# Performance work log

Hardware: AMD Instinct MI355X
Metric: run time of the kernel (lower is better)

## Reference

```python
import jax, jax.numpy as jnp
import numpy as np
from jax import lax

# dims per init_kwargs / input_specs
V, D, N, W, B, T = 32000, 512, 250000, 64, 4, 1024
LOOPS, THRESH = 4, 0.99


def _ln(x, scale, bias):
    m = jnp.mean(x, -1, keepdims=True)
    v = jnp.var(x, -1, keepdims=True)
    return (x - m) * lax.rsqrt(v + 1e-5) * scale + bias


def setup_inputs() -> dict:
    key = jax.random.key(0)
    ks = jax.random.split(key, 12)
    s = 0.02
    p = lambda k, shape: jax.random.normal(k, shape, jnp.float32) * s
    return {
        "input_ids": jax.random.randint(ks[0], (B, T), 0, V),
        "embed": p(ks[1], (V, D)),
        "enc_w": p(ks[2], (D, D)), "enc_b": jnp.zeros((D,), jnp.float32),
        "ln_enc_s": jnp.ones((D,), jnp.float32), "ln_enc_b": jnp.zeros((D,), jnp.float32),
        "idx_w": p(ks[3], (D, D)), "idx_b": jnp.zeros((D,), jnp.float32),
        "mu_w": p(ks[4], (D, 1)), "mu_b": jnp.zeros((1,), jnp.float32),
        "sig_w": p(ks[5], (D, 1)), "sig_b": jnp.zeros((1,), jnp.float32),
        "pool_table": p(ks[6], (N, D)),
        "int_w1": p(ks[7], (2 * D, D)), "int_b1": jnp.zeros((D,), jnp.float32),
        "int_w2": p(ks[8], (D, D)), "int_b2": jnp.zeros((D,), jnp.float32),
        "ln_s": jnp.ones((D,), jnp.float32), "ln_b": jnp.zeros((D,), jnp.float32),
        "halt_w": p(ks[9], (D, 1)), "halt_b": jnp.zeros((1,), jnp.float32),
        "dec_w": p(ks[10], (D, V)), "dec_b": jnp.zeros((V,), jnp.float32),
    }


def reference(input_ids, embed, enc_w, enc_b, ln_enc_s, ln_enc_b,
              idx_w, idx_b, mu_w, mu_b, sig_w, sig_b, pool_table,
              int_w1, int_b1, int_w2, int_b2, ln_s, ln_b,
              halt_w, halt_b, dec_w, dec_b):
    # TinyController.encode: embed -> Dense -> gelu -> LayerNorm
    hidden = _ln(jax.nn.gelu(embed[input_ids] @ enc_w + enc_b), ln_enc_s, ln_enc_b)  # [B,T,D]
    state = hidden
    dt = hidden.dtype
    halt_prob = jnp.zeros((B, T, 1), dt)
    halted = jnp.zeros((B, T, 1), dt)
    idxs = []
    for _ in range(LOOPS):  # fixed small loop count, unrolled
        prev = state
        pooled = jnp.mean(state, axis=1)                       # [B,D]
        h = jax.nn.gelu(pooled @ idx_w + idx_b)
        mu = jax.nn.sigmoid(h @ mu_w + mu_b)                   # [B,1], coord in [0,1]
        sigma = jax.nn.softplus(h @ sig_w + sig_b) + 1e-4      # [B,1]
        # CoordinateMassivePool: contiguous window of W rows around mu*N
        center = mu[:, 0] * N
        start = jnp.clip(jnp.floor(center - W / 2).astype(jnp.int32), 0, N - W)  # [B]
        window = jax.vmap(lambda s: lax.dynamic_slice(pool_table, (s, 0), (W, D)))(start)  # [B,W,D]
        pos = (start[:, None] + jnp.arange(W)[None, :]).astype(dt) / N            # [B,W]
        w = jnp.exp(-0.5 * ((pos - mu) / sigma) ** 2)
        w = w / jnp.sum(w, axis=-1, keepdims=True)
        retrieved = jnp.einsum('bw,bwd->bd', w, window)        # [B,D]
        combined = jnp.concatenate(
            [state, jnp.broadcast_to(retrieved[:, None, :], (B, T, D))], axis=-1)  # [B,T,2D]
        integrated = _ln(jax.nn.gelu(combined @ int_w1 + int_b1) @ int_w2 + int_b2, ln_s, ln_b)
        candidate = state + integrated
        # ACT halting
        p_halt = jax.nn.sigmoid(candidate @ halt_w + halt_b)   # [B,T,1]
        halt_prob = halt_prob + p_halt * (1.0 - halted)
        new_halted = (halt_prob > THRESH).astype(dt)
        state = (1.0 - halted) * candidate + halted * prev
        halted = new_halted
        idxs.append(start)
    logits = state @ dec_w + dec_b                             # [B,T,V]
    all_indices = jnp.stack(idxs, axis=1)                      # [B,LOOPS]
    return logits, all_indices
```

## Files before the change

### kernel.cpp

```cpp
#include <hip/hip_runtime.h>

#define DEV __device__ __forceinline__

typedef __attribute__((ext_vector_type(8))) short bf16x8;
typedef __attribute__((ext_vector_type(4))) float f32x4;

typedef const __attribute__((address_space(1))) void* gsrc_t;
typedef __attribute__((address_space(3))) void* gdst_t;

DEV void gld16(const void* g, void* l){ __builtin_amdgcn_global_load_lds((gsrc_t)g,(gdst_t)l,16,0,0); }

DEV unsigned short f2bf(float f){
  union { float f; unsigned int u; } x; x.f = f;
  unsigned int u = x.u;
  return (unsigned short)((u + 0x7fffu + ((u >> 16) & 1u)) >> 16);
}
DEV unsigned long long pack4bf(float a, float b, float c, float d){
  return (unsigned long long)f2bf(a)
       | ((unsigned long long)f2bf(b) << 16)
       | ((unsigned long long)f2bf(c) << 32)
       | ((unsigned long long)f2bf(d) << 48);
}
DEV float gelu_t(float x){
  float u = 0.7978845608028654f * (x + 0.044715f * x * x * x);
  return 0.5f * x * (1.0f + tanhf(u));
}
DEV float sigmoidf_(float x){ return 1.0f / (1.0f + expf(-x)); }

DEV void BAR_TOP(){ __builtin_amdgcn_s_barrier(); asm volatile("" ::: "memory"); }
DEV void BAR_END(){
  __builtin_amdgcn_sched_barrier(0);
  asm volatile("s_waitcnt lgkmcnt(0)" ::: "memory");
  __builtin_amdgcn_s_barrier();
  asm volatile("" ::: "memory");
}

__global__ __launch_bounds__(256) void kPrep(const float* __restrict__ dec_w,
                                             unsigned short* __restrict__ dec_wT,
                                             const float* __restrict__ s0, const float* __restrict__ s1,
                                             const float* __restrict__ s2,
                                             unsigned short* __restrict__ d0, unsigned short* __restrict__ d1,
                                             unsigned short* __restrict__ d2,
                                             const int* __restrict__ ids,
                                             const float* __restrict__ embed,
                                             unsigned short* __restrict__ E){
  __shared__ float t[64][65];
  const int bid = blockIdx.x, tid = threadIdx.x;
  if (bid < 4000){
    int n0 = (bid % 500) * 64, k0 = (bid / 500) * 64;
    #pragma unroll
    for (int i = 0; i < 16; i++){
      int idx = i * 256 + tid; int r = idx >> 6, c = idx & 63;
      t[r][c] = dec_w[(size_t)(k0 + r) * 32000 + n0 + c];
    }
    __syncthreads();
    #pragma unroll
    for (int i = 0; i < 16; i++){
      int idx = i * 256 + tid; int r = idx >> 6, c = idx & 63;
      dec_wT[(size_t)(n0 + r) * 512 + k0 + c] = f2bf(t[c][r]);
    }
  } else if (bid < 4192){
    int rel = bid - 4000;
    int z = rel >> 6, rem = rel & 63;
    const float* W = (z == 0) ? s0 : (z == 1) ? s1 : s2;
    unsigned short* D = (z == 0) ? d0 : (z == 1) ? d1 : d2;
    int n0 = (rem & 7) * 64, k0 = (rem >> 3) * 64;
    #pragma unroll
    for (int i = 0; i < 16; i++){
      int idx = i * 256 + tid; int r = idx >> 6, c = idx & 63;
      t[r][c] = W[(size_t)(k0 + r) * 512 + n0 + c];
    }
    __syncthreads();
    #pragma unroll
    for (int i = 0; i < 16; i++){
      int idx = i * 256 + tid; int r = idx >> 6, c = idx & 63;
      D[(size_t)(n0 + r) * 512 + k0 + c] = f2bf(t[c][r]);
    }
  } else {
    int idx = bid - 4192;
    int row = idx * 2 + (tid >> 7);
    int t2  = tid & 127;
    int id = ids[row];
    float4 v = ((const float4*)(embed + (size_t)id * 512))[t2];
    *(unsigned long long*)(E + (size_t)row * 512 + t2 * 4) = pack4bf(v.x, v.y, v.z, v.w);
  }
}

template<int ENC>
__global__ __launch_bounds__(512) void kGemmLN(
    const unsigned short* __restrict__ A, const unsigned short* __restrict__ BT,
    const float* __restrict__ bias, const float* __restrict__ lns, const float* __restrict__ lnb,
    const float* __restrict__ hw, const float* __restrict__ hb,
    float* __restrict__ st, unsigned short* __restrict__ stb,
    float* __restrict__ part, float* __restrict__ halt_p, float* __restrict__ halted){
  __shared__ alignas(16) unsigned short lA[2][16 * 32];
  __shared__ alignas(16) unsigned short lB[2][512 * 32];
  __shared__ float pS[8][16], pQ[8][16], pH[8][16];
  __shared__ float sMean[16], sRs[16], sFac[16];
  const int tid = threadIdx.x, w = tid >> 6, lane = tid & 63;
  const int q = lane >> 4, c = lane & 15, lk8 = q * 8;
  const int r0 = blockIdx.x * 16;
  const int br = tid >> 2, bk = (tid & 3) * 8;
  f32x4 acc[4] = {};

  auto STAGE = [&](int buf, int k0){
    if (w == 0)
      gld16(A + (size_t)(r0 + (lane >> 2)) * 512 + k0 + (lane & 3) * 8, &lA[buf][lane * 8]);
    #pragma unroll
    for (int i = 0; i < 4; i++)
      gld16(BT + (size_t)(i * 128 + br) * 512 + k0 + bk, &lB[buf][(i * 512 + tid) * 8]);
  };

  STAGE(0, 0);
  #pragma unroll
  for (int t = 0; t < 16; t++){
    if (t < 15){
      STAGE((t + 1) & 1, (t + 1) * 32);
      if (w == 0) asm volatile("s_waitcnt vmcnt(5)" ::: "memory");
      else        asm volatile("s_waitcnt vmcnt(4)" ::: "memory");
    } else {
      asm volatile("s_waitcnt vmcnt(0)" ::: "memory");
    }
    BAR_TOP();
    bf16x8 af = *(const bf16x8*)&lA[t & 1][c * 32 + lk8];
    bf16x8 bfv[4];
    #pragma unroll
    for (int n = 0; n < 4; n++)
      bfv[n] = *(const bf16x8*)&lB[t & 1][(w * 64 + n * 16 + c) * 32 + lk8];
    #pragma unroll
    for (int n = 0; n < 4; n++)
      acc[n] = __builtin_amdgcn_mfma_f32_16x16x32_bf16(af, bfv[n], acc[n], 0, 0, 0);
    BAR_END();
  }

  #pragma unroll
  for (int n = 0; n < 4; n++){
    float bcol = bias[w * 64 + n * 16 + c];
    #pragma unroll
    for (int r = 0; r < 4; r++){
      float v = acc[n][r] + bcol;
      if (ENC) v = gelu_t(v);
      acc[n][r] = v;
    }
  }
  float rS[4], rQ[4];
  #pragma unroll
  for (int r = 0; r < 4; r++){
    float s = 0.f, s2 = 0.f;
    #pragma unroll
    for (int n = 0; n < 4; n++){ float v = acc[n][r]; s += v; s2 += v * v; }
    rS[r] = s; rQ[r] = s2;
  }
  #pragma unroll
  for (int mask = 1; mask < 16; mask <<= 1)
    #pragma unroll
    for (int r = 0; r < 4; r++){
      rS[r] += __shfl_xor(rS[r], mask);
      rQ[r] += __shfl_xor(rQ[r], mask);
    }
  if (c == 0)
    #pragma unroll
    for (int r = 0; r < 4; r++){ pS[w][q * 4 + r] = rS[r]; pQ[w][q * 4 + r] = rQ[r]; }
  __syncthreads();
  if (tid < 16){
    float s = 0.f, s2 = 0.f;
    #pragma unroll
    for (int v = 0; v < 8; v++){ s += pS[v][tid]; s2 += pQ[v][tid]; }
    float mean = s * (1.f / 512.f);
    float var  = s2 * (1.f / 512.f) - mean * mean;
    sMean[tid] = mean; sRs[tid] = rsqrtf(var + 1e-5f);
    if (ENC){ halt_p[r0 + tid] = 0.f; halted[r0 + tid] = 0.f; }
  }
  __syncthreads();
  float lnsv[4], lnbv[4];
  #pragma unroll
  for (int n = 0; n < 4; n++){ lnsv[n] = lns[w * 64 + n * 16 + c]; lnbv[n] = lnb[w * 64 + n * 16 + c]; }
  #pragma unroll
  for (int r = 0; r < 4; r++){
    int row = q * 4 + r;
    float mu = sMean[row], rs = sRs[row];
    #pragma unroll
    for (int n = 0; n < 4; n++)
      acc[n][r] = (acc[n][r] - mu) * rs * lnsv[n] + lnbv[n];
  }

  float sold[4][4];
  if (!ENC){
    float hwv[4];
    #pragma unroll
    for (int n = 0; n < 4; n++) hwv[n] = hw[w * 64 + n * 16 + c];
    #pragma unroll
    for (int r = 0; r < 4; r++){
      int row = q * 4 + r;
      #pragma unroll
      for (int n = 0; n < 4; n++)
        sold[n][r] = st[(size_t)(r0 + row) * 512 + w * 64 + n * 16 + c];
    }
    float rH[4];
    #pragma unroll
    for (int r = 0; r < 4; r++){
      float d = 0.f;
      #pragma unroll
      for (int n = 0; n < 4; n++) d += (sold[n][r] + acc[n][r]) * hwv[n];
      rH[r] = d;
    }
    #pragma unroll
    for (int mask = 1; mask < 16; mask <<= 1)
      #pragma unroll
      for (int r = 0; r < 4; r++) rH[r] += __shfl_xor(rH[r], mask);
    if (c == 0)
      #pragma unroll
      for (int r = 0; r < 4; r++) pH[w][q * 4 + r] = rH[r];
    __syncthreads();
    if (tid < 16){
      float d = 0.f;
      #pragma unroll
      for (int v = 0; v < 8; v++) d += pH[v][tid];
      float hd = halted[r0 + tid];
      float p  = sigmoidf_(d + hb[0]);
      float hp = halt_p[r0 + tid] + p * (1.f - hd);
      halt_p[r0 + tid] = hp;
      halted[r0 + tid] = (hp > 0.99f) ? 1.f : 0.f;
      sFac[tid] = 1.f - hd;
    }
    __syncthreads();
    #pragma unroll
    for (int r = 0; r < 4; r++){
      float f = sFac[q * 4 + r];
      #pragma unroll
      for (int n = 0; n < 4; n++)
        acc[n][r] = sold[n][r] + f * acc[n][r];
    }
  }

  #pragma unroll
  for (int r = 0; r < 4; r++){
    int row = r0 + q * 4 + r;
    #pragma unroll
    for (int n = 0; n < 4; n++){
      int col = w * 64 + n * 16 + c;
      float v = acc[n][r];
      st [(size_t)row * 512 + col] = v;
      stb[(size_t)row * 512 + col] = f2bf(v);
    }
  }
  #pragma unroll
  for (int n = 0; n < 4; n++){
    float s = 0.f;
    #pragma unroll
    for (int r = 0; r < 4; r++) s += acc[n][r];
    s += __shfl_xor(s, 16);
    s += __shfl_xor(s, 32);
    if (q == 0) part[(size_t)blockIdx.x * 512 + w * 64 + n * 16 + c] = s;
  }
}

__global__ __launch_bounds__(256) void kGemm64(const unsigned short* __restrict__ A,
                                               const unsigned short* __restrict__ BT,
                                               const float* __restrict__ rb,
                                               unsigned short* __restrict__ C){
  __shared__ alignas(16) unsigned short lA[2][64 * 32];
  __shared__ alignas(16) unsigned short lB[2][64 * 32];
  const int tid = threadIdx.x, w = tid >> 6, lane = tid & 63;
  const int q = lane >> 4, c = lane & 15, lk8 = q * 8;
  const int wm = w >> 1, wn = w & 1;
  const int m0 = blockIdx.y * 64, n0 = blockIdx.x * 64;
  const int sr = tid >> 2, sk = (tid & 3) * 8;
  f32x4 acc[2][2] = {};

  auto STAGE = [&](int buf, int k0){
    gld16(A  + (size_t)(m0 + sr) * 512 + k0 + sk, &lA[buf][tid * 8]);
    gld16(BT + (size_t)(n0 + sr) * 512 + k0 + sk, &lB[buf][tid * 8]);
  };

  STAGE(0, 0);
  #pragma unroll
  for (int t = 0; t < 16; t++){
    if (t < 15){
      STAGE((t + 1) & 1, (t + 1) * 32);
      asm volatile("s_waitcnt vmcnt(2)" ::: "memory");
    } else {
      asm volatile("s_waitcnt vmcnt(0)" ::: "memory");
    }
    BAR_TOP();
    bf16x8 af[2], bfv[2];
    #pragma unroll
    for (int m = 0; m < 2; m++) af[m]  = *(const bf16x8*)&lA[t & 1][(wm * 32 + m * 16 + c) * 32 + lk8];
    #pragma unroll
    for (int n = 0; n < 2; n++) bfv[n] = *(const bf16x8*)&lB[t & 1][(wn * 32 + n * 16 + c) * 32 + lk8];
    #pragma unroll
    for (int m = 0; m < 2; m++)
      #pragma unroll
      for (int n = 0; n < 2; n++)
        acc[m][n] = __builtin_amdgcn_mfma_f32_16x16x32_bf16(af[m], bfv[n], acc[m][n], 0, 0, 0);
    BAR_END();
  }

  #pragma unroll
  for (int m = 0; m < 2; m++)
    #pragma unroll
    for (int n = 0; n < 2; n++)
      #pragma unroll
      for (int r = 0; r < 4; r++){
        int row = m0 + wm * 32 + m * 16 + q * 4 + r;
        int col = n0 + wn * 32 + n * 16 + c;
        float v = acc[m][n][r] + rb[((row >> 10) << 9) + col];
        C[(size_t)row * 512 + col] = f2bf(gelu_t(v));
      }
}

__global__ __launch_bounds__(256) void kGemmDec(const unsigned short* __restrict__ A,
                                                const unsigned short* __restrict__ BT,
                                                const float* __restrict__ bias,
                                                float* __restrict__ C){
  __shared__ alignas(16) unsigned short lA[3][128 * 32];
  __shared__ alignas(16) unsigned short lB[3][128 * 32];
  const int tid = threadIdx.x, w = tid >> 6, lane = tid & 63;
  const int wm = w >> 1, wn = w & 1;
  const int c = lane & 15, q = lane >> 4;
  const int rk8 = (q ^ ((c >> 1) & 3)) * 8;
  int flat = blockIdx.x;
  flat = (flat & 7) * 1000 + (flat >> 3);
  const int m0 = (flat & 31) * 128;
  const int n0 = (flat >> 5) * 128;
  const int srow  = tid >> 2;
  const int skoff = ((tid & 3) ^ ((srow >> 1) & 3)) * 8;
  const int sdst  = srow * 32 + (tid & 3) * 8;
  f32x4 acc[4][4] = {};

  auto STAGE = [&](int buf, int k0){
    gld16(A  + (size_t)(m0 + srow) * 512 + k0 + skoff,      &lA[buf][sdst]);
    gld16(A  + (size_t)(m0 + 64 + srow) * 512 + k0 + skoff, &lA[buf][64 * 32 + sdst]);
    gld16(BT + (size_t)(n0 + srow) * 512 + k0 + skoff,      &lB[buf][sdst]);
    gld16(BT + (size_t)(n0 + 64 + srow) * 512 + k0 + skoff, &lB[buf][64 * 32 + sdst]);
  };

  STAGE(0, 0);
  STAGE(1, 32);
  for (int t = 0; t < 16; t++){
    const int buf = t % 3;
    if (t < 15) asm volatile("s_waitcnt vmcnt(4)" ::: "memory");
    else        asm volatile("s_waitcnt vmcnt(0)" ::: "memory");
    __builtin_amdgcn_s_barrier();
    asm volatile("" ::: "memory");
    bf16x8 af[4], bfr[4];
    #pragma unroll
    for (int mf = 0; mf < 4; mf++)
      af[mf] = *(const bf16x8*)&lA[buf][(wm * 64 + mf * 16 + c) * 32 + rk8];
    #pragma unroll
    for (int nf = 0; nf < 4; nf++)
      bfr[nf] = *(const bf16x8*)&lB[buf][(wn * 64 + nf * 16 + c) * 32 + rk8];
    if (t < 14) STAGE((t + 2) % 3, (t + 2) * 32);
    asm volatile("s_waitcnt lgkmcnt(0)" ::: "memory");
    __builtin_amdgcn_sched_barrier(0);
    __builtin_amdgcn_s_setprio(1);
    #pragma unroll
    for (int mf = 0; mf < 4; mf++)
      #pragma unroll
      for (int nf = 0; nf < 4; nf++)
        acc[mf][nf] = __builtin_amdgcn_mfma_f32_16x16x32_bf16(af[mf], bfr[nf], acc[mf][nf], 0, 0, 0);
    __builtin_amdgcn_s_setprio(0);
  }

  #pragma unroll
  for (int mf = 0; mf < 4; mf++){
    int rbase = m0 + wm * 64 + mf * 16 + q * 4;
    #pragma unroll
    for (int nf = 0; nf < 4; nf++){
      int col = n0 + wn * 64 + nf * 16 + c;
      float bcol = bias[col];
      #pragma unroll
      for (int r = 0; r < 4; r++)
        __builtin_nontemporal_store(acc[mf][nf][r] + bcol,
                                    &C[(size_t)(rbase + r) * 32000 + col]);
    }
  }
}

__global__ __launch_bounds__(512) void kCtl(const float* __restrict__ part,
                                            const float* __restrict__ idx_w, const float* __restrict__ idx_b,
                                            const float* __restrict__ mu_w, const float* __restrict__ mu_b,
                                            const float* __restrict__ sig_w, const float* __restrict__ sig_b,
                                            const float* __restrict__ pool_table,
                                            const float* __restrict__ w1b, const float* __restrict__ int_b1,
                                            float* __restrict__ r2, float* __restrict__ outIdx, int loop){
  __shared__ float xs[512];
  __shared__ float red[512];
  __shared__ float red2[512];
  __shared__ float evals[64];
  __shared__ float sc[4];
  int b = blockIdx.x, tid = threadIdx.x;

  float s = 0.f;
  #pragma unroll 8
  for (int c2 = 0; c2 < 64; c2++) s += part[(size_t)(b * 64 + c2) * 512 + tid];
  xs[tid] = s * (1.0f / 1024.0f);
  __syncthreads();

  float a = idx_b[tid];
  #pragma unroll 16
  for (int i = 0; i < 512; i++)
    a = fmaf(xs[i], idx_w[(size_t)i * 512 + tid], a);
  float hv = gelu_t(a);
  red[tid]  = hv * mu_w[tid];
  red2[tid] = hv * sig_w[tid];
  __syncthreads();
  for (int off2 = 256; off2 > 0; off2 >>= 1){
    if (tid < off2){ red[tid] += red[tid + off2]; red2[tid] += red2[tid + off2]; }
    __syncthreads();
  }
  if (tid == 0){
    float mu = sigmoidf_(red[0] + mu_b[0]);
    float sg = log1pf(expf(red2[0] + sig_b[0])) + 1e-4f;
    float center = mu * 250000.0f;
    int stt = (int)floorf(center - 32.0f);
    stt = stt < 0 ? 0 : (stt > 250000 - 64 ? 250000 - 64 : stt);
    sc[0] = mu; sc[1] = sg; sc[2] = (float)stt;
    outIdx[b * 4 + loop] = (float)stt;
  }
  __syncthreads();
  if (tid < 64){
    float pos = (sc[2] + (float)tid) * (1.0f / 250000.0f);
    float z = (pos - sc[0]) / sc[1];
    evals[tid] = expf(-0.5f * z * z);
  }
  __syncthreads();
  if (tid == 0){
    float wsum = 0.f;
    for (int j = 0; j < 64; j++) wsum += evals[j];
    sc[3] = wsum;
  }
  __syncthreads();
  int stt = (int)sc[2];
  float r = 0.f;
  #pragma unroll 8
  for (int j = 0; j < 64; j++)
    r = fmaf(evals[j], pool_table[(size_t)(stt + j) * 512 + tid], r);
  r /= sc[3];
  __syncthreads();
  xs[tid] = r;
  __syncthreads();
  float a2 = int_b1[tid];
  #pragma unroll 16
  for (int i = 0; i < 512; i++)
    a2 = fmaf(xs[i], w1b[(size_t)i * 512 + tid], a2);
  r2[(size_t)b * 512 + tid] = a2;
}

extern "C" void kernel_launch(void* const* d_in, const int* in_sizes, int n_in,
                              void* d_out, int out_size, void* d_ws, size_t ws_size,
                              hipStream_t stream){
  (void)in_sizes; (void)n_in; (void)out_size; (void)ws_size;
  const int*   ids    = (const int*)  d_in[0];
  const float* embed  = (const float*)d_in[1];
  const float* enc_w  = (const float*)d_in[2];
  const float* enc_b  = (const float*)d_in[3];
  const float* ln_es  = (const float*)d_in[4];
  const float* ln_eb  = (const float*)d_in[5];
  const float* idx_w  = (const float*)d_in[6];
  const float* idx_b  = (const float*)d_in[7];
  const float* mu_w   = (const float*)d_in[8];
  const float* mu_b   = (const float*)d_in[9];
  const float* sig_w  = (const float*)d_in[10];
  const float* sig_b  = (const float*)d_in[11];
  const float* pool_t = (const float*)d_in[12];
  const float* int_w1 = (const float*)d_in[13];
  const float* int_b1 = (const float*)d_in[14];
  const float* int_w2 = (const float*)d_in[15];
  const float* int_b2 = (const float*)d_in[16];
  const float* ln_s   = (const float*)d_in[17];
  const float* ln_b   = (const float*)d_in[18];
  const float* halt_w = (const float*)d_in[19];
  const float* halt_b = (const float*)d_in[20];
  const float* dec_w  = (const float*)d_in[21];
  const float* dec_b  = (const float*)d_in[22];

  char* ws = (char*)d_ws;
  size_t off = 0;
  auto alloc = [&](size_t bytes)->char*{
    char* p = ws + off; off += (bytes + 255) & ~(size_t)255; return p;
  };
  unsigned short* dec_wT  = (unsigned short*)alloc(32000ull * 512 * 2);
  unsigned short* enc_wT  = (unsigned short*)alloc(512ull * 512 * 2);
  unsigned short* w1T     = (unsigned short*)alloc(512ull * 512 * 2);
  unsigned short* w2T     = (unsigned short*)alloc(512ull * 512 * 2);
  unsigned short* bufB    = (unsigned short*)alloc(4096ull * 512 * 2);
  float*          state   = (float*)alloc(4096ull * 512 * 4);
  unsigned short* state_b = (unsigned short*)alloc(4096ull * 512 * 2);
  float*          part    = (float*)alloc(256ull * 512 * 4);
  float*          r2      = (float*)alloc(4ull * 512 * 4);
  float*          halt_p  = (float*)alloc(4096 * 4);
  float*          halted  = (float*)alloc(4096 * 4);
  float*          outF    = (float*)d_out;

  hipLaunchKernelGGL(kPrep, dim3(6240), dim3(256), 0, stream,
                     dec_w, dec_wT, enc_w, int_w1, int_w2, enc_wT, w1T, w2T,
                     ids, embed, bufB);

  hipLaunchKernelGGL((kGemmLN<1>), dim3(256), dim3(512), 0, stream,
                     bufB, enc_wT, enc_b, ln_es, ln_eb,
                     (const float*)nullptr, (const float*)nullptr,
                     state, state_b, part, halt_p, halted);

  for (int l = 0; l < 4; l++){
    hipLaunchKernelGGL(kCtl, dim3(4), dim3(512), 0, stream, part, idx_w, idx_b,
                       mu_w, mu_b, sig_w, sig_b, pool_t,
                       int_w1 + 512 * 512, int_b1,
                       r2, outF + 131072000, l);
    hipLaunchKernelGGL(kGemm64, dim3(8, 64), dim3(256), 0, stream,
                       state_b, w1T, r2, bufB);
    hipLaunchKernelGGL((kGemmLN<0>), dim3(256), dim3(512), 0, stream,
                       bufB, w2T, int_b2, ln_s, ln_b, halt_w, halt_b,
                       state, state_b, part, halt_p, halted);
  }

  hipLaunchKernelGGL(kGemmDec, dim3(8000), dim3(256), 0, stream,
                     state_b, dec_wT, dec_b, (float*)d_out);
}
```

Baseline: 507.7 us.

## Fuse the two integrator GEMMs into one kernel with the hidden tile kept in LDS

Merges the first integrator GEMM (state × W1 + retrieved bias, then gelu) and the second GEMM with LayerNorm and halting into a single kernel, kLoop. Each block computes a 16-row intermediate tile, stores it as bf16 in shared memory, and feeds it straight into the second GEMM. This removes one launch per loop iteration and the global round trip of the 4096x512 intermediate. The cost is that every 16-row block now streams all of W1 as well as W2, which raises weight traffic per block, and the first GEMM now runs with only 256 blocks of 512 threads.

Result: slower. 521.0 us (+2.6%).

```diff
diff --git a/kernel.cpp b/kernel.cpp
--- a/kernel.cpp
+++ b/kernel.cpp
@@ -86,17 +86,15 @@
   }
 }
 
-template<int ENC>
-__global__ __launch_bounds__(512) void kGemmLN(
+__global__ __launch_bounds__(512) void kEnc(
     const unsigned short* __restrict__ A, const unsigned short* __restrict__ BT,
     const float* __restrict__ bias, const float* __restrict__ lns, const float* __restrict__ lnb,
-    const float* __restrict__ hw, const float* __restrict__ hb,
     float* __restrict__ st, unsigned short* __restrict__ stb,
     float* __restrict__ part, float* __restrict__ halt_p, float* __restrict__ halted){
   __shared__ alignas(16) unsigned short lA[2][16 * 32];
   __shared__ alignas(16) unsigned short lB[2][512 * 32];
-  __shared__ float pS[8][16], pQ[8][16], pH[8][16];
-  __shared__ float sMean[16], sRs[16], sFac[16];
+  __shared__ float pS[8][16], pQ[8][16];
+  __shared__ float sMean[16], sRs[16];
   const int tid = threadIdx.x, w = tid >> 6, lane = tid & 63;
   const int q = lane >> 4, c = lane & 15, lk8 = q * 8;
   const int r0 = blockIdx.x * 16;
@@ -137,11 +135,8 @@
   for (int n = 0; n < 4; n++){
     float bcol = bias[w * 64 + n * 16 + c];
     #pragma unroll
-    for (int r = 0; r < 4; r++){
-      float v = acc[n][r] + bcol;
-      if (ENC) v = gelu_t(v);
-      acc[n][r] = v;
-    }
+    for (int r = 0; r < 4; r++)
+      acc[n][r] = gelu_t(acc[n][r] + bcol);
   }
   float rS[4], rQ[4];
   #pragma unroll
@@ -169,7 +164,7 @@
     float mean = s * (1.f / 512.f);
     float var  = s2 * (1.f / 512.f) - mean * mean;
     sMean[tid] = mean; sRs[tid] = rsqrtf(var + 1e-5f);
-    if (ENC){ halt_p[r0 + tid] = 0.f; halted[r0 + tid] = 0.f; }
+    halt_p[r0 + tid] = 0.f; halted[r0 + tid] = 0.f;
   }
   __syncthreads();
   float lnsv[4], lnbv[4];
@@ -183,56 +178,6 @@
     for (int n = 0; n < 4; n++)
       acc[n][r] = (acc[n][r] - mu) * rs * lnsv[n] + lnbv[n];
   }
-
-  float sold[4][4];
-  if (!ENC){
-    float hwv[4];
-    #pragma unroll
-    for (int n = 0; n < 4; n++) hwv[n] = hw[w * 64 + n * 16 + c];
-    #pragma unroll
-    for (int r = 0; r < 4; r++){
-      int row = q * 4 + r;
-      #pragma unroll
-      for (int n = 0; n < 4; n++)
-        sold[n][r] = st[(size_t)(r0 + row) * 512 + w * 64 + n * 16 + c];
-    }
-    float rH[4];
-    #pragma unroll
-    for (int r = 0; r < 4; r++){
-      float d = 0.f;
-      #pragma unroll
-      for (int n = 0; n < 4; n++) d += (sold[n][r] + acc[n][r]) * hwv[n];
-      rH[r] = d;
-    }
-    #pragma unroll
-    for (int mask = 1; mask < 16; mask <<= 1)
-      #pragma unroll
-      for (int r = 0; r < 4; r++) rH[r] += __shfl_xor(rH[r], mask);
-    if (c == 0)
-      #pragma unroll
-      for (int r = 0; r < 4; r++) pH[w][q * 4 + r] = rH[r];
-    __syncthreads();
-    if (tid < 16){
-      float d = 0.f;
-      #pragma unroll
-      for (int v = 0; v < 8; v++) d += pH[v][tid];
-      float hd = halted[r0 + tid];
-      float p  = sigmoidf_(d + hb[0]);
-      float hp = halt_p[r0 + tid] + p * (1.f - hd);
-      halt_p[r0 + tid] = hp;
-      halted[r0 + tid] = (hp > 0.99f) ? 1.f : 0.f;
-      sFac[tid] = 1.f - hd;
-    }
-    __syncthreads();
-    #pragma unroll
-    for (int r = 0; r < 4; r++){
-      float f = sFac[q * 4 + r];
-      #pragma unroll
-      for (int n = 0; n < 4; n++)
-        acc[n][r] = sold[n][r] + f * acc[n][r];
-    }
-  }
-
   #pragma unroll
   for (int r = 0; r < 4; r++){
     int row = r0 + q * 4 + r;
@@ -255,58 +200,209 @@
   }
 }
 
-__global__ __launch_bounds__(256) void kGemm64(const unsigned short* __restrict__ A,
-                                               const unsigned short* __restrict__ BT,
-                                               const float* __restrict__ rb,
-                                               unsigned short* __restrict__ C){
-  __shared__ alignas(16) unsigned short lA[2][64 * 32];
-  __shared__ alignas(16) unsigned short lB[2][64 * 32];
+__global__ __launch_bounds__(512) void kLoop(
+    const unsigned short* __restrict__ A,
+    const unsigned short* __restrict__ W1T, const unsigned short* __restrict__ W2T,
+    const float* __restrict__ r2, const float* __restrict__ b2,
+    const float* __restrict__ lns, const float* __restrict__ lnb,
+    const float* __restrict__ hw, const float* __restrict__ hb,
+    float* __restrict__ st, unsigned short* __restrict__ stb,
+    float* __restrict__ part, float* __restrict__ halt_p, float* __restrict__ halted){
+  __shared__ alignas(16) unsigned short lA[2][16 * 32];
+  __shared__ alignas(16) unsigned short lB[2][512 * 32];
+  __shared__ alignas(16) unsigned short G[16 * 516];
+  __shared__ float pS[8][16], pQ[8][16], pH[8][16];
+  __shared__ float sMean[16], sRs[16], sFac[16];
   const int tid = threadIdx.x, w = tid >> 6, lane = tid & 63;
   const int q = lane >> 4, c = lane & 15, lk8 = q * 8;
-  const int wm = w >> 1, wn = w & 1;
-  const int m0 = blockIdx.y * 64, n0 = blockIdx.x * 64;
-  const int sr = tid >> 2, sk = (tid & 3) * 8;
-  f32x4 acc[2][2] = {};
-
-  auto STAGE = [&](int buf, int k0){
-    gld16(A  + (size_t)(m0 + sr) * 512 + k0 + sk, &lA[buf][tid * 8]);
-    gld16(BT + (size_t)(n0 + sr) * 512 + k0 + sk, &lB[buf][tid * 8]);
+  const int r0 = blockIdx.x * 16;
+  const int b = blockIdx.x >> 6;
+  const int br = tid >> 2, bk = (tid & 3) * 8;
+
+  float4 rbv[4];
+  #pragma unroll
+  for (int mt = 0; mt < 4; mt++)
+    rbv[mt] = *(const float4*)(r2 + b * 512 + w * 64 + mt * 16 + q * 4);
+  asm volatile("s_waitcnt vmcnt(0)" ::: "memory");
+
+  auto STG_B = [&](int buf, const unsigned short* W, int k0){
+    #pragma unroll
+    for (int i = 0; i < 4; i++)
+      gld16(W + (size_t)(i * 128 + br) * 512 + k0 + bk, &lB[buf][(i * 512 + tid) * 8]);
   };
-
-  STAGE(0, 0);
+  auto STG_A = [&](int buf, int k0){
+    if (w == 0)
+      gld16(A + (size_t)(r0 + (lane >> 2)) * 512 + k0 + (lane & 3) * 8, &lA[buf][lane * 8]);
+  };
+
+  f32x4 acc1[4] = {};
+  STG_A(0, 0); STG_B(0, W1T, 0);
   #pragma unroll
   for (int t = 0; t < 16; t++){
     if (t < 15){
-      STAGE((t + 1) & 1, (t + 1) * 32);
-      asm volatile("s_waitcnt vmcnt(2)" ::: "memory");
+      STG_A((t + 1) & 1, (t + 1) * 32);
+      STG_B((t + 1) & 1, W1T, (t + 1) * 32);
+      if (w == 0) asm volatile("s_waitcnt vmcnt(5)" ::: "memory");
+      else        asm volatile("s_waitcnt vmcnt(4)" ::: "memory");
+    } else {
+      STG_B(0, W2T, 0);
+      asm volatile("s_waitcnt vmcnt(4)" ::: "memory");
+    }
+    BAR_TOP();
+    bf16x8 bfs = *(const bf16x8*)&lA[t & 1][c * 32 + lk8];
+    bf16x8 afw[4];
+    #pragma unroll
+    for (int mt = 0; mt < 4; mt++)
+      afw[mt] = *(const bf16x8*)&lB[t & 1][(w * 64 + mt * 16 + c) * 32 + lk8];
+    #pragma unroll
+    for (int mt = 0; mt < 4; mt++)
+      acc1[mt] = __builtin_amdgcn_mfma_f32_16x16x32_bf16(afw[mt], bfs, acc1[mt], 0, 0, 0);
+    BAR_END();
+  }
+
+  #pragma unroll
+  for (int mt = 0; mt < 4; mt++){
+    float v0 = gelu_t(acc1[mt][0] + rbv[mt].x);
+    float v1 = gelu_t(acc1[mt][1] + rbv[mt].y);
+    float v2 = gelu_t(acc1[mt][2] + rbv[mt].z);
+    float v3 = gelu_t(acc1[mt][3] + rbv[mt].w);
+    *(unsigned long long*)&G[c * 516 + w * 64 + mt * 16 + q * 4] = pack4bf(v0, v1, v2, v3);
+  }
+  BAR_END();
+
+  f32x4 acc[4] = {};
+  #pragma unroll
+  for (int t = 0; t < 16; t++){
+    if (t < 15){
+      STG_B((t + 1) & 1, W2T, (t + 1) * 32);
+      asm volatile("s_waitcnt vmcnt(4)" ::: "memory");
     } else {
       asm volatile("s_waitcnt vmcnt(0)" ::: "memory");
     }
     BAR_TOP();
-    bf16x8 af[2], bfv[2];
-    #pragma unroll
-    for (int m = 0; m < 2; m++) af[m]  = *(const bf16x8*)&lA[t & 1][(wm * 32 + m * 16 + c) * 32 + lk8];
-    #pragma unroll
-    for (int n = 0; n < 2; n++) bfv[n] = *(const bf16x8*)&lB[t & 1][(wn * 32 + n * 16 + c) * 32 + lk8];
-    #pragma unroll
-    for (int m = 0; m < 2; m++)
-      #pragma unroll
-      for (int n = 0; n < 2; n++)
-        acc[m][n] = __builtin_amdgcn_mfma_f32_16x16x32_bf16(af[m], bfv[n], acc[m][n], 0, 0, 0);
+    bf16x8 afg = *(const bf16x8*)&G[c * 516 + t * 32 + lk8];
+    bf16x8 bfw[4];
+    #pragma unroll
+    for (int n = 0; n < 4; n++)
+      bfw[n] = *(const bf16x8*)&lB[t & 1][(w * 64 + n * 16 + c) * 32 + lk8];
+    #pragma unroll
+    for (int n = 0; n < 4; n++)
+      acc[n] = __builtin_amdgcn_mfma_f32_16x16x32_bf16(afg, bfw[n], acc[n], 0, 0, 0);
     BAR_END();
   }
 
   #pragma unroll
-  for (int m = 0; m < 2; m++)
-    #pragma unroll
-    for (int n = 0; n < 2; n++)
-      #pragma unroll
-      for (int r = 0; r < 4; r++){
-        int row = m0 + wm * 32 + m * 16 + q * 4 + r;
-        int col = n0 + wn * 32 + n * 16 + c;
-        float v = acc[m][n][r] + rb[((row >> 10) << 9) + col];
-        C[(size_t)row * 512 + col] = f2bf(gelu_t(v));
-      }
+  for (int n = 0; n < 4; n++){
+    float bcol = b2[w * 64 + n * 16 + c];
+    #pragma unroll
+    for (int r = 0; r < 4; r++) acc[n][r] += bcol;
+  }
+  float rS[4], rQ[4];
+  #pragma unroll
+  for (int r = 0; r < 4; r++){
+    float s = 0.f, s2 = 0.f;
+    #pragma unroll
+    for (int n = 0; n < 4; n++){ float v = acc[n][r]; s += v; s2 += v * v; }
+    rS[r] = s; rQ[r] = s2;
+  }
+  #pragma unroll
+  for (int mask = 1; mask < 16; mask <<= 1)
+    #pragma unroll
+    for (int r = 0; r < 4; r++){
+      rS[r] += __shfl_xor(rS[r], mask);
+      rQ[r] += __shfl_xor(rQ[r], mask);
+    }
+  if (c == 0)
+    #pragma unroll
+    for (int r = 0; r < 4; r++){ pS[w][q * 4 + r] = rS[r]; pQ[w][q * 4 + r] = rQ[r]; }
+  __syncthreads();
+  if (tid < 16){
+    float s = 0.f, s2 = 0.f;
+    #pragma unroll
+    for (int v = 0; v < 8; v++){ s += pS[v][tid]; s2 += pQ[v][tid]; }
+    float mean = s * (1.f / 512.f);
+    float var  = s2 * (1.f / 512.f) - mean * mean;
+    sMean[tid] = mean; sRs[tid] = rsqrtf(var + 1e-5f);
+  }
+  __syncthreads();
+  float lnsv[4], lnbv[4], hwv[4];
+  #pragma unroll
+  for (int n = 0; n < 4; n++){
+    lnsv[n] = lns[w * 64 + n * 16 + c];
+    lnbv[n] = lnb[w * 64 + n * 16 + c];
+    hwv[n]  = hw [w * 64 + n * 16 + c];
+  }
+  #pragma unroll
+  for (int r = 0; r < 4; r++){
+    int row = q * 4 + r;
+    float mu = sMean[row], rs = sRs[row];
+    #pragma unroll
+    for (int n = 0; n < 4; n++)
+      acc[n][r] = (acc[n][r] - mu) * rs * lnsv[n] + lnbv[n];
+  }
+  float sold[4][4];
+  #pragma unroll
+  for (int r = 0; r < 4; r++){
+    int row = q * 4 + r;
+    #pragma unroll
+    for (int n = 0; n < 4; n++)
+      sold[n][r] = st[(size_t)(r0 + row) * 512 + w * 64 + n * 16 + c];
+  }
+  float rH[4];
+  #pragma unroll
+  for (int r = 0; r < 4; r++){
+    float d = 0.f;
+    #pragma unroll
+    for (int n = 0; n < 4; n++) d += (sold[n][r] + acc[n][r]) * hwv[n];
+    rH[r] = d;
+  }
+  #pragma unroll
+  for (int mask = 1; mask < 16; mask <<= 1)
+    #pragma unroll
+    for (int r = 0; r < 4; r++) rH[r] += __shfl_xor(rH[r], mask);
+  if (c == 0)
+    #pragma unroll
+    for (int r = 0; r < 4; r++) pH[w][q * 4 + r] = rH[r];
+  __syncthreads();
+  if (tid < 16){
+    float d = 0.f;
+    #pragma unroll
+    for (int v = 0; v < 8; v++) d += pH[v][tid];
+    float hd = halted[r0 + tid];
+    float p  = sigmoidf_(d + hb[0]);
+    float hp = halt_p[r0 + tid] + p * (1.f - hd);
+    halt_p[r0 + tid] = hp;
+    halted[r0 + tid] = (hp > 0.99f) ? 1.f : 0.f;
+    sFac[tid] = 1.f - hd;
+  }
+  __syncthreads();
+  #pragma unroll
+  for (int r = 0; r < 4; r++){
+    float f = sFac[q * 4 + r];
+    #pragma unroll
+    for (int n = 0; n < 4; n++)
+      acc[n][r] = sold[n][r] + f * acc[n][r];
+  }
+  #pragma unroll
+  for (int r = 0; r < 4; r++){
+    int row = r0 + q * 4 + r;
+    #pragma unroll
+    for (int n = 0; n < 4; n++){
+      int col = w * 64 + n * 16 + c;
+      float v = acc[n][r];
+      st [(size_t)row * 512 + col] = v;
+      stb[(size_t)row * 512 + col] = f2bf(v);
+    }
+  }
+  #pragma unroll
+  for (int n = 0; n < 4; n++){
+    float s = 0.f;
+    #pragma unroll
+    for (int r = 0; r < 4; r++) s += acc[n][r];
+    s += __shfl_xor(s, 16);
+    s += __shfl_xor(s, 32);
+    if (q == 0) part[(size_t)blockIdx.x * 512 + w * 64 + n * 16 + c] = s;
+  }
 }
 
 __global__ __launch_bounds__(256) void kGemmDec(const unsigned short* __restrict__ A,
@@ -497,9 +593,8 @@
                      dec_w, dec_wT, enc_w, int_w1, int_w2, enc_wT, w1T, w2T,
                      ids, embed, bufB);
 
-  hipLaunchKernelGGL((kGemmLN<1>), dim3(256), dim3(512), 0, stream,
+  hipLaunchKernelGGL(kEnc, dim3(256), dim3(512), 0, stream,
                      bufB, enc_wT, enc_b, ln_es, ln_eb,
-                     (const float*)nullptr, (const float*)nullptr,
                      state, state_b, part, halt_p, halted);
 
   for (int l = 0; l < 4; l++){
@@ -507,10 +602,8 @@
                        mu_w, mu_b, sig_w, sig_b, pool_t,
                        int_w1 + 512 * 512, int_b1,
                        r2, outF + 131072000, l);
-    hipLaunchKernelGGL(kGemm64, dim3(8, 64), dim3(256), 0, stream,
-                       state_b, w1T, r2, bufB);
-    hipLaunchKernelGGL((kGemmLN<0>), dim3(256), dim3(512), 0, stream,
-                       bufB, w2T, int_b2, ln_s, ln_b, halt_w, halt_b,
+    hipLaunchKernelGGL(kLoop, dim3(256), dim3(512), 0, stream,
+                       state_b, w1T, w2T, r2, int_b2, ln_s, ln_b, halt_w, halt_b,
                        state, state_b, part, halt_p, halted);
   }
 
```
